# Kernel tuning notes

Hardware: AMD Instinct MI355X
Metric: run time of the kernel (lower is better)

Reference implementation:

```python
import jax, jax.numpy as jnp
import numpy as np

OFFSET = 3  # windows 3,5,7


def _maxpool_same(x, k):
    # MaxPool2d(kernel=k, stride=1, padding=(k-1)//2); torch pads with -inf
    p = (k - 1) // 2
    return jax.lax.reduce_window(
        x, -jnp.inf, jax.lax.max,
        window_dimensions=(1, 1, k, k),
        window_strides=(1, 1, 1, 1),
        padding=((0, 0), (0, 0), (p, p), (p, p)))


def setup_inputs() -> dict:
    key = jax.random.key(0)
    # strictly positive so log10 is finite
    x = jax.random.uniform(key, (8, 64, 256, 256), dtype=jnp.float32,
                           minval=1e-3, maxval=1.0)
    return {"x": x}


def reference(x) -> jnp.ndarray:
    B, C, H, W = x.shape
    windows = jnp.array([2.0 * i + 1.0 for i in range(1, OFFSET + 1)],
                        dtype=x.dtype)  # [3,5,7]
    xs = jnp.log10(windows / (H * W))
    xc = xs - xs.mean()
    # Closed-form OLS slope weights: inv(X X^T) X reduces analytically to
    # w_i = (x_i - xbar) / sum_j (x_j - xbar)^2 for the slope row.
    w = xc / jnp.sum(xc * xc)                  # [OFFSET]
    # slope = sum_i w_i * log10(maxpool_{k_i}(x)), computed without stacking
    holder = jnp.zeros_like(x)
    for i in range(OFFSET):
        k = 2 * (i + 1) + 1
        holder = holder + w[i] * jnp.log10(_maxpool_same(x, k))
    return holder  # (B, C, H, W)
```

## Files before the change

kernel.cpp:

```cpp
#include <hip/hip_runtime.h>
#include <cmath>


#define IMG_H 256
#define IMG_W 256
#define RPW   16
#define PF    4

typedef float vfloat4 __attribute__((ext_vector_type(4)));

__device__ __forceinline__ float dpp_left(float v) {
  return __int_as_float(
      __builtin_amdgcn_update_dpp(0, __float_as_int(v), 0x138, 0xF, 0xF, true));
}
__device__ __forceinline__ float dpp_right(float v) {
  return __int_as_float(
      __builtin_amdgcn_update_dpp(0, __float_as_int(v), 0x130, 0xF, 0xF, true));
}

__device__ __forceinline__ float4 f4max(float4 a, float4 b) {
  return make_float4(fmaxf(a.x, b.x), fmaxf(a.y, b.y),
                     fmaxf(a.z, b.z), fmaxf(a.w, b.w));
}

struct PS { float p1, p2, p3, s1, s2, s3, f; };

__device__ __forceinline__ PS make_ps(float4 a) {
  PS r;
  r.p1 = a.x;
  r.p2 = fmaxf(a.x, a.y);
  r.p3 = fmaxf(r.p2, a.z);
  r.s1 = a.w;
  r.s2 = fmaxf(a.z, a.w);
  r.s3 = fmaxf(a.y, r.s2);
  r.f  = fmaxf(r.p2, r.s2);
  return r;
}

__global__ __launch_bounds__(256, 4) void holder_kernel(
    const float* __restrict__ x, float* __restrict__ out,
    float w3, float w5, float w7)
{
  const int lane = threadIdx.x & 63;
  const int wave = threadIdx.x >> 6;
  const int img  = blockIdx.x;
  const int band = blockIdx.y;
  const int r0   = band * (4 * RPW) + wave * RPW;

  const float* px = x   + (size_t)img * (IMG_H * IMG_W) + lane * 4;
  float*       po = out + (size_t)img * (IMG_H * IMG_W) + lane * 4;

  const float4 zero = make_float4(0.f, 0.f, 0.f, 0.f);

  float4 win[7 + PF];
#pragma unroll
  for (int i = 0; i < 7 + PF; ++i) {
    int rr = r0 - 3 + i;
    win[i] = (rr >= 0 && rr < IMG_H) ? *(const float4*)(px + rr * IMG_W) : zero;
  }

#pragma unroll 4
  for (int r = r0; r < r0 + RPW; ++r) {
    int rn = r + 4 + PF;
    float4 nxt = (rn < IMG_H && (rn - r0) < RPW + 3)
                     ? *(const float4*)(px + rn * IMG_W) : zero;

    float4 v1 = f4max(f4max(win[2], win[3]), win[4]);
    float4 v2 = f4max(v1, f4max(win[1], win[5]));
    float4 v3 = f4max(v2, f4max(win[0], win[6]));

    PS a1 = make_ps(v1), a2 = make_ps(v2), a3 = make_ps(v3);

    float L1s1 = dpp_left(a1.s1);
    float L2s1 = dpp_left(a2.s1);
    float L2s2 = dpp_left(a2.s2);
    float L3s1 = dpp_left(a3.s1);
    float L3s2 = dpp_left(a3.s2);
    float L3s3 = dpp_left(a3.s3);

    float R1p1 = dpp_right(a1.p1);
    float R2p1 = dpp_right(a2.p1);
    float R2p2 = dpp_right(a2.p2);
    float R3p1 = dpp_right(a3.p1);
    float R3p2 = dpp_right(a3.p2);
    float R3p3 = dpp_right(a3.p3);

    float m3_0 = fmaxf(L1s1, a1.p2);
    float m3_1 = a1.p3;
    float m3_2 = a1.s3;
    float m3_3 = fmaxf(a1.s2, R1p1);

    float m5_0 = fmaxf(L2s2, a2.p3);
    float m5_1 = fmaxf(L2s1, a2.f);
    float m5_2 = fmaxf(a2.f, R2p1);
    float m5_3 = fmaxf(a2.s3, R2p2);

    float m7_0 = fmaxf(L3s3, a3.f);
    float m7_1 = fmaxf(fmaxf(L3s2, a3.f), R3p1);
    float m7_2 = fmaxf(fmaxf(L3s1, a3.f), R3p2);
    float m7_3 = fmaxf(a3.f, R3p3);

    vfloat4 o;
    o.x = fmaf(w7, __log2f(m7_0), fmaf(w5, __log2f(m5_0), w3 * __log2f(m3_0)));
    o.y = fmaf(w7, __log2f(m7_1), fmaf(w5, __log2f(m5_1), w3 * __log2f(m3_1)));
    o.z = fmaf(w7, __log2f(m7_2), fmaf(w5, __log2f(m5_2), w3 * __log2f(m3_2)));
    o.w = fmaf(w7, __log2f(m7_3), fmaf(w5, __log2f(m5_3), w3 * __log2f(m3_3)));
    __builtin_nontemporal_store(o, (vfloat4*)(po + r * IMG_W));

#pragma unroll
    for (int i = 0; i < 6 + PF; ++i) win[i] = win[i + 1];
    win[6 + PF] = nxt;
  }
}

extern "C" void kernel_launch(void* const* d_in, const int* in_sizes, int n_in,
                              void* d_out, int out_size, void* d_ws, size_t ws_size,
                              hipStream_t stream) {
  const float* x = (const float*)d_in[0];
  float* out = (float*)d_out;

  const int n_img = in_sizes[0] / (IMG_H * IMG_W);

  const double l0 = log10(3.0), l1 = log10(5.0), l2 = log10(7.0);
  const double m  = (l0 + l1 + l2) / 3.0;
  const double c0 = l0 - m, c1 = l1 - m, c2 = l2 - m;
  const double s  = c0 * c0 + c1 * c1 + c2 * c2;
  const double LG2 = 0.30102999566398119521;
  const float w3 = (float)(c0 / s * LG2);
  const float w5 = (float)(c1 / s * LG2);
  const float w7 = (float)(c2 / s * LG2);

  hipLaunchKernelGGL(holder_kernel, dim3(n_img, 4), dim3(256), 0, stream,
                     x, out, w3, w5, w7);
}
```

Before: 246.4 us.

## Software-pipeline row loads in chunks with inline-asm loads and explicit waitcnt

Replaces the per-row sliding prefetch with a chunked scheme. Four future rows are issued as raw global_load_dwordx4 via inline asm, four output rows are computed and stored, and then an explicit s_waitcnt vmcnt(4) waits for the loads. Out-of-range rows are clamped to valid addresses and zeroed after the wait, which removes the branches around the loads. The goal is to keep more loads in flight and hide memory latency in this bandwidth-bound stencil. The cost is that correctness relies on the hand-written vmcnt accounting, including the stores that count toward vmcnt on this architecture.

```diff
diff --git a/kernel.cpp b/kernel.cpp
--- a/kernel.cpp
+++ b/kernel.cpp
@@ -5,9 +5,29 @@
 #define IMG_H 256
 #define IMG_W 256
 #define RPW   16
-#define PF    4
+#define CH    4
 
-typedef float vfloat4 __attribute__((ext_vector_type(4)));
+typedef float vf4 __attribute__((ext_vector_type(4)));
+
+__device__ __forceinline__ vf4 aload(const float* base, uint32_t voff) {
+  vf4 r;
+  asm volatile("global_load_dwordx4 %0, %1, %2"
+               : "=v"(r) : "v"(voff), "s"(base) : "memory");
+  return r;
+}
+
+__device__ __forceinline__ void wait4(vf4& a, vf4& b, vf4& c, vf4& d) {
+  asm volatile("s_waitcnt vmcnt(4)"
+               : "+v"(a), "+v"(b), "+v"(c), "+v"(d) :: "memory");
+}
+
+__device__ __forceinline__ void wait0_10(vf4& a, vf4& b, vf4& c, vf4& d,
+                                         vf4& e, vf4& f, vf4& g, vf4& h,
+                                         vf4& i, vf4& j) {
+  asm volatile("s_waitcnt vmcnt(0)"
+               : "+v"(a), "+v"(b), "+v"(c), "+v"(d), "+v"(e),
+                 "+v"(f), "+v"(g), "+v"(h), "+v"(i), "+v"(j) :: "memory");
+}
 
 __device__ __forceinline__ float dpp_left(float v) {
   return __int_as_float(
@@ -18,14 +38,16 @@
       __builtin_amdgcn_update_dpp(0, __float_as_int(v), 0x130, 0xF, 0xF, true));
 }
 
-__device__ __forceinline__ float4 f4max(float4 a, float4 b) {
-  return make_float4(fmaxf(a.x, b.x), fmaxf(a.y, b.y),
-                     fmaxf(a.z, b.z), fmaxf(a.w, b.w));
+__device__ __forceinline__ vf4 vmax(vf4 a, vf4 b) {
+  vf4 r;
+  r.x = fmaxf(a.x, b.x); r.y = fmaxf(a.y, b.y);
+  r.z = fmaxf(a.z, b.z); r.w = fmaxf(a.w, b.w);
+  return r;
 }
 
 struct PS { float p1, p2, p3, s1, s2, s3, f; };
 
-__device__ __forceinline__ PS make_ps(float4 a) {
+__device__ __forceinline__ PS make_ps(vf4 a) {
   PS r;
   r.p1 = a.x;
   r.p2 = fmaxf(a.x, a.y);
@@ -47,69 +69,94 @@
   const int band = blockIdx.y;
   const int r0   = band * (4 * RPW) + wave * RPW;
 
-  const float* px = x   + (size_t)img * (IMG_H * IMG_W) + lane * 4;
+  const float* px = x + (size_t)img * (IMG_H * IMG_W);
   float*       po = out + (size_t)img * (IMG_H * IMG_W) + lane * 4;
+  const uint32_t lo = (uint32_t)lane * 16u;
 
-  const float4 zero = make_float4(0.f, 0.f, 0.f, 0.f);
+  const vf4 vzero = (vf4)0.0f;
 
-  float4 win[7 + PF];
+  vf4 w[10];
 #pragma unroll
-  for (int i = 0; i < 7 + PF; ++i) {
+  for (int i = 0; i < 10; ++i) {
     int rr = r0 - 3 + i;
-    win[i] = (rr >= 0 && rr < IMG_H) ? *(const float4*)(px + rr * IMG_W) : zero;
+    int rc = rr < 0 ? 0 : (rr > IMG_H - 1 ? IMG_H - 1 : rr);
+    w[i] = aload(px, (uint32_t)(rc * IMG_W * 4) + lo);
+  }
+  wait0_10(w[0], w[1], w[2], w[3], w[4], w[5], w[6], w[7], w[8], w[9]);
+#pragma unroll
+  for (int i = 0; i < 10; ++i) {
+    int rr = r0 - 3 + i;
+    if (rr < 0 || rr >= IMG_H) w[i] = vzero;
   }
 
-#pragma unroll 4
-  for (int r = r0; r < r0 + RPW; ++r) {
-    int rn = r + 4 + PF;
-    float4 nxt = (rn < IMG_H && (rn - r0) < RPW + 3)
-                     ? *(const float4*)(px + rn * IMG_W) : zero;
+#pragma unroll
+  for (int c = 0; c < RPW / CH; ++c) {
+    const int R = r0 + c * CH;
 
-    float4 v1 = f4max(f4max(win[2], win[3]), win[4]);
-    float4 v2 = f4max(v1, f4max(win[1], win[5]));
-    float4 v3 = f4max(v2, f4max(win[0], win[6]));
-
-    PS a1 = make_ps(v1), a2 = make_ps(v2), a3 = make_ps(v3);
-
-    float L1s1 = dpp_left(a1.s1);
-    float L2s1 = dpp_left(a2.s1);
-    float L2s2 = dpp_left(a2.s2);
-    float L3s1 = dpp_left(a3.s1);
-    float L3s2 = dpp_left(a3.s2);
-    float L3s3 = dpp_left(a3.s3);
-
-    float R1p1 = dpp_right(a1.p1);
-    float R2p1 = dpp_right(a2.p1);
-    float R2p2 = dpp_right(a2.p2);
-    float R3p1 = dpp_right(a3.p1);
-    float R3p2 = dpp_right(a3.p2);
-    float R3p3 = dpp_right(a3.p3);
-
-    float m3_0 = fmaxf(L1s1, a1.p2);
-    float m3_1 = a1.p3;
-    float m3_2 = a1.s3;
-    float m3_3 = fmaxf(a1.s2, R1p1);
-
-    float m5_0 = fmaxf(L2s2, a2.p3);
-    float m5_1 = fmaxf(L2s1, a2.f);
-    float m5_2 = fmaxf(a2.f, R2p1);
-    float m5_3 = fmaxf(a2.s3, R2p2);
-
-    float m7_0 = fmaxf(L3s3, a3.f);
-    float m7_1 = fmaxf(fmaxf(L3s2, a3.f), R3p1);
-    float m7_2 = fmaxf(fmaxf(L3s1, a3.f), R3p2);
-    float m7_3 = fmaxf(a3.f, R3p3);
-
-    vfloat4 o;
-    o.x = fmaf(w7, __log2f(m7_0), fmaf(w5, __log2f(m5_0), w3 * __log2f(m3_0)));
-    o.y = fmaf(w7, __log2f(m7_1), fmaf(w5, __log2f(m5_1), w3 * __log2f(m3_1)));
-    o.z = fmaf(w7, __log2f(m7_2), fmaf(w5, __log2f(m5_2), w3 * __log2f(m3_2)));
-    o.w = fmaf(w7, __log2f(m7_3), fmaf(w5, __log2f(m5_3), w3 * __log2f(m3_3)));
-    __builtin_nontemporal_store(o, (vfloat4*)(po + r * IMG_W));
+    vf4 nw[CH];
+#pragma unroll
+    for (int j = 0; j < CH; ++j) {
+      int rr = R + 7 + j;
+      int rc = rr > IMG_H - 1 ? IMG_H - 1 : rr;
+      nw[j] = aload(px, (uint32_t)(rc * IMG_W * 4) + lo);
+    }
 
 #pragma unroll
-    for (int i = 0; i < 6 + PF; ++i) win[i] = win[i + 1];
-    win[6 + PF] = nxt;
+    for (int j = 0; j < CH; ++j) {
+      vf4 v1 = vmax(vmax(w[j + 2], w[j + 3]), w[j + 4]);
+      vf4 v2 = vmax(v1, vmax(w[j + 1], w[j + 5]));
+      vf4 v3 = vmax(v2, vmax(w[j + 0], w[j + 6]));
+
+      PS a1 = make_ps(v1), a2 = make_ps(v2), a3 = make_ps(v3);
+
+      float L1s1 = dpp_left(a1.s1);
+      float L2s1 = dpp_left(a2.s1);
+      float L2s2 = dpp_left(a2.s2);
+      float L3s1 = dpp_left(a3.s1);
+      float L3s2 = dpp_left(a3.s2);
+      float L3s3 = dpp_left(a3.s3);
+
+      float R1p1 = dpp_right(a1.p1);
+      float R2p1 = dpp_right(a2.p1);
+      float R2p2 = dpp_right(a2.p2);
+      float R3p1 = dpp_right(a3.p1);
+      float R3p2 = dpp_right(a3.p2);
+      float R3p3 = dpp_right(a3.p3);
+
+      float m3_0 = fmaxf(L1s1, a1.p2);
+      float m3_1 = a1.p3;
+      float m3_2 = a1.s3;
+      float m3_3 = fmaxf(a1.s2, R1p1);
+
+      float m5_0 = fmaxf(L2s2, a2.p3);
+      float m5_1 = fmaxf(L2s1, a2.f);
+      float m5_2 = fmaxf(a2.f, R2p1);
+      float m5_3 = fmaxf(a2.s3, R2p2);
+
+      float m7_0 = fmaxf(L3s3, a3.f);
+      float m7_1 = fmaxf(fmaxf(L3s2, a3.f), R3p1);
+      float m7_2 = fmaxf(fmaxf(L3s1, a3.f), R3p2);
+      float m7_3 = fmaxf(a3.f, R3p3);
+
+      vf4 o;
+      o.x = fmaf(w7, __log2f(m7_0), fmaf(w5, __log2f(m5_0), w3 * __log2f(m3_0)));
+      o.y = fmaf(w7, __log2f(m7_1), fmaf(w5, __log2f(m5_1), w3 * __log2f(m3_1)));
+      o.z = fmaf(w7, __log2f(m7_2), fmaf(w5, __log2f(m5_2), w3 * __log2f(m3_2)));
+      o.w = fmaf(w7, __log2f(m7_3), fmaf(w5, __log2f(m5_3), w3 * __log2f(m3_3)));
+      __builtin_nontemporal_store(o, (vf4*)(po + (R + j) * IMG_W));
+    }
+
+    wait4(nw[0], nw[1], nw[2], nw[3]);
+
+#pragma unroll
+    for (int j = 0; j < CH; ++j) {
+      int rr = R + 7 + j;
+      if (rr >= IMG_H) nw[j] = vzero;
+    }
+#pragma unroll
+    for (int i = 0; i < 10 - CH; ++i) w[i] = w[i + CH];
+#pragma unroll
+    for (int j = 0; j < CH; ++j) w[10 - CH + j] = nw[j];
   }
 }
 
```

New measurement: 234.1 us. 5.0% less time.
